# Kernel tuning notes

Hardware: AMD Instinct MI355X
Metric: run time of the kernel (lower is better)

Reference implementation:

```python
import jax, jax.numpy as jnp
import numpy as np

IN_F, OUT_F, K = 1024, 1024, 12
EPS = 1e-6


def setup_inputs() -> dict:
    key = jax.random.key(0)
    k1, k2, k3, k4 = jax.random.split(key, 4)
    x = jax.random.normal(k1, (4, 4096, IN_F), dtype=jnp.float32)
    # grid: linspace(-2,2,K) per feature + small noise so sort is nontrivial
    base = jnp.linspace(-2.0, 2.0, K, dtype=jnp.float32)
    grid = base[None, :] + 0.1 * jax.random.normal(k2, (IN_F, K), dtype=jnp.float32)
    coeffs = 0.1 * jax.random.normal(k3, (IN_F, K), dtype=jnp.float32)
    tangents = jnp.zeros((IN_F, K), dtype=jnp.float32)
    knot_alive = jnp.full((IN_F, K), 3.0, dtype=jnp.float32)
    kw1, kw2 = jax.random.split(k4)
    proj_w = jax.random.normal(kw1, (OUT_F, IN_F), dtype=jnp.float32) / np.sqrt(IN_F)
    proj_b = jnp.zeros((OUT_F,), dtype=jnp.float32)
    res_w = jax.random.normal(kw2, (OUT_F, IN_F), dtype=jnp.float32) / np.sqrt(IN_F)
    return {"x": x, "grid": grid, "coeffs": coeffs, "tangents": tangents,
            "knot_alive": knot_alive, "proj_w": proj_w, "proj_b": proj_b, "res_w": res_w}


def _eval_hermite_spline(x, grid, coeffs, tangents, knot_alive):
    # sort knots per input feature (grid: [F,K])
    sort_idx = jnp.argsort(grid, axis=1)
    sorted_grid = jnp.take_along_axis(grid, sort_idx, axis=1)
    sorted_coeffs = jnp.take_along_axis(coeffs, sort_idx, axis=1)
    sorted_tangents = jnp.take_along_axis(tangents, sort_idx, axis=1)
    sorted_alive = jnp.take_along_axis(knot_alive, sort_idx, axis=1)
    alive = jax.nn.sigmoid(sorted_alive)
    mc = sorted_coeffs * alive          # masked heights [F,K]
    mt = sorted_tangents * alive        # masked tangents [F,K]

    orig_shape = x.shape
    xf = x.reshape(-1, orig_shape[-1])  # [M,F]
    gmin = sorted_grid[:, 0]            # [F]
    gmax = sorted_grid[:, -1]
    xc = jnp.clip(xf, gmin[None, :], gmax[None, :])
    grange = jnp.maximum(gmax - gmin, EPS)
    xn = (xc - gmin[None, :]) / grange[None, :] * (K - 1)  # [M,F]
    idx_l = jnp.clip(xn.astype(jnp.int32), 0, K - 2)
    t = xn - idx_l.astype(xf.dtype)

    feat = jnp.arange(xf.shape[1])[None, :]  # [1,F] broadcast against [M,F] idx
    p0 = mc[feat, idx_l]
    p1 = mc[feat, idx_l + 1]
    m0 = mt[feat, idx_l]
    m1 = mt[feat, idx_l + 1]
    x_left = sorted_grid[feat, idx_l]
    x_right = sorted_grid[feat, idx_l + 1]
    dx = jnp.maximum(x_right - x_left, EPS)

    t2 = t * t
    t3 = t2 * t
    h00 = 2 * t3 - 3 * t2 + 1
    h10 = t3 - 2 * t2 + t
    h01 = -2 * t3 + 3 * t2
    h11 = t3 - t2
    out = h00 * p0 + h10 * m0 * dx + h01 * p1 + h11 * m1 * dx
    return out.reshape(orig_shape)


def reference(x, grid, coeffs, tangents, knot_alive, proj_w, proj_b, res_w):
    spline_out = _eval_hermite_spline(x, grid, coeffs, tangents, knot_alive)
    # proj(spline_out) + residual(x); torch Linear: y = x @ W.T + b
    return (jnp.einsum('...i,oi->...o', spline_out, proj_w) + proj_b
            + jnp.einsum('...i,oi->...o', x, res_w))
```

## Files before the change

### kernel.cpp

```cpp
#include <hip/hip_runtime.h>
#include <hip/hip_bf16.h>


#define IN_F   1024
#define OUT_F  1024
#define KNOTS  12
#define M_ROWS 16384
#define GK     2048

#define BM   256
#define BN   256
#define BKT  64
#define NTK  (GK / BKT)

typedef __attribute__((ext_vector_type(8))) __bf16 bf16x8;
typedef __attribute__((ext_vector_type(4))) float  f32x4;

__device__ __forceinline__ unsigned short f2bf(float v) {
    unsigned int u = __float_as_uint(v);
    u = (u + 0x7fffu + ((u >> 16) & 1u)) >> 16;
    return (unsigned short)u;
}

__device__ __forceinline__ void gload16(const void* g, void* l) {
    __builtin_amdgcn_global_load_lds(
        (const __attribute__((address_space(1))) void*)g,
        (__attribute__((address_space(3))) void*)l, 16, 0, 0);
}

__global__ __launch_bounds__(256) void prep_kernel(
    const float* __restrict__ grid, const float* __restrict__ coeffs,
    const float* __restrict__ tangents, const float* __restrict__ alive,
    float* __restrict__ gmin, float* __restrict__ scale, float4* __restrict__ H)
{
    int f = blockIdx.x * blockDim.x + threadIdx.x;
    if (f >= IN_F) return;
    float g[KNOTS], c[KNOTS], t[KNOTS], a[KNOTS];
    for (int i = 0; i < KNOTS; ++i) {
        g[i] = grid[f*KNOTS+i];  c[i] = coeffs[f*KNOTS+i];
        t[i] = tangents[f*KNOTS+i]; a[i] = alive[f*KNOTS+i];
    }
    for (int i = 1; i < KNOTS; ++i) {
        float gk=g[i], ck=c[i], tk=t[i], ak=a[i];
        int j = i-1;
        while (j >= 0 && g[j] > gk) { g[j+1]=g[j]; c[j+1]=c[j]; t[j+1]=t[j]; a[j+1]=a[j]; --j; }
        g[j+1]=gk; c[j+1]=ck; t[j+1]=tk; a[j+1]=ak;
    }
    float mcl[KNOTS], mtl[KNOTS];
    for (int i = 0; i < KNOTS; ++i) {
        float s = 1.f / (1.f + expf(-a[i]));
        mcl[i] = c[i]*s;  mtl[i] = t[i]*s;
    }
    gmin[f] = g[0];
    float grange = fmaxf(g[KNOTS-1] - g[0], 1e-6f);
    scale[f] = (float)(KNOTS-1) / grange;
    for (int k = 0; k < KNOTS-1; ++k) {
        float dx = fmaxf(g[k+1]-g[k], 1e-6f);
        H[(size_t)f*KNOTS + k] = make_float4(mcl[k], mcl[k+1], mtl[k]*dx, mtl[k+1]*dx);
    }
    H[(size_t)f*KNOTS + KNOTS-1] = make_float4(0.f, 0.f, 0.f, 0.f);
}

#define SROWS 64
#define HPAD  13
__global__ __launch_bounds__(256) void spline_kernel(const float* __restrict__ x,
    const float* __restrict__ gmin, const float* __restrict__ scale,
    const float4* __restrict__ H, unsigned short* __restrict__ A)
{
    __shared__ float4 sH[256 * HPAD];
    __shared__ float  sGm[256], sSc[256];
    const int tid  = threadIdx.x;
    const int fblk = blockIdx.y * 256;
    #pragma unroll
    for (int k = 0; k < KNOTS; ++k) sH[tid*HPAD + k] = H[(size_t)(fblk+tid)*KNOTS + k];
    sGm[tid] = gmin[fblk+tid];
    sSc[tid] = scale[fblk+tid];
    __syncthreads();

    const int wave = tid >> 6, lane = tid & 63;
    const int f0 = lane * 4;
    const float4 gm4 = *reinterpret_cast<const float4*>(&sGm[f0]);
    const float4 sc4 = *reinterpret_cast<const float4*>(&sSc[f0]);
    const float gms[4] = {gm4.x, gm4.y, gm4.z, gm4.w};
    const float scs[4] = {sc4.x, sc4.y, sc4.z, sc4.w};
    const int r0 = blockIdx.x * SROWS;

    #pragma unroll 8
    for (int r = wave; r < SROWS; r += 4) {
        const int row = r0 + r;
        const float4 xv = *reinterpret_cast<const float4*>(x + (size_t)row*IN_F + fblk + f0);
        const float xs[4] = {xv.x, xv.y, xv.z, xv.w};
        ushort4 so, xo;
        unsigned short* sp = (unsigned short*)&so;
        unsigned short* xp = (unsigned short*)&xo;
        #pragma unroll
        for (int j = 0; j < 4; ++j) {
            const float xi = xs[j];
            float xn = (xi - gms[j]) * scs[j];
            xn = fminf(fmaxf(xn, 0.f), (float)(KNOTS-1));
            int idx = (int)xn;  idx = idx > (KNOTS-2) ? (KNOTS-2) : idx;
            const float tt = xn - (float)idx;
            const float4 h = sH[(f0+j)*HPAD + idx];
            const float t2 = tt*tt, t3 = t2*tt;
            const float h00 =  2.f*t3 - 3.f*t2 + 1.f;
            const float h01 = -2.f*t3 + 3.f*t2;
            const float h10 =  t3 - 2.f*t2 + tt;
            const float h11 =  t3 - t2;
            sp[j] = f2bf(h00*h.x + h01*h.y + h10*h.z + h11*h.w);
            xp[j] = f2bf(xi);
        }
        const size_t base = (size_t)row * GK + fblk + f0;
        *reinterpret_cast<ushort4*>(A + base)        = so;
        *reinterpret_cast<ushort4*>(A + base + IN_F) = xo;
    }
}

__global__ __launch_bounds__(256) void bcast_kernel(
    const float* __restrict__ P, const float* __restrict__ R,
    unsigned short* __restrict__ Bc)
{
    int g = blockIdx.x*256 + threadIdx.x;
    int n  = g >> 9;
    int k4 = (g & 511) * 4;
    const float* src = (k4 < IN_F) ? (P + (size_t)n*IN_F + k4)
                                   : (R + (size_t)n*IN_F + (k4 - IN_F));
    float4 v = *reinterpret_cast<const float4*>(src);
    ushort4 o;
    o.x = f2bf(v.x); o.y = f2bf(v.y); o.z = f2bf(v.z); o.w = f2bf(v.w);
    *reinterpret_cast<ushort4*>(Bc + (size_t)n*GK + k4) = o;
}

__global__ __launch_bounds__(1024, 4) void gemm_kernel(
    const unsigned short* __restrict__ A, const unsigned short* __restrict__ B,
    const float* __restrict__ bias, float* __restrict__ C)
{
    __shared__ unsigned short sA[2][BM*BKT];
    __shared__ unsigned short sB[2][BN*BKT];

    const int tid  = threadIdx.x;
    const int wg   = blockIdx.x;
    const int swzb = (wg & 7) * 32 + (wg >> 3);
    const int by   = swzb >> 2;
    const int bx   = swzb & 3;

    const int lane = tid & 63;
    const int wave = tid >> 6;
    const int wm   = wave >> 2;
    const int wn   = wave & 3;
    const int lr   = lane & 15;
    const int lsl  = lane >> 4;

    const size_t aRow0 = (size_t)by * BM;
    const size_t bRow0 = (size_t)bx * BN;

    auto stage = [&](const unsigned short* __restrict__ G, size_t gRow0,
                     unsigned short* lds, int ts) {
        const int k0 = ts * BKT;
        #pragma unroll
        for (int i = 0; i < 2; ++i) {
            const int L16  = i*1024 + tid;
            const int lrow = L16 >> 3;
            const int ss   = (L16 & 7) ^ (lrow & 7);
            gload16(G + (gRow0 + lrow)*GK + k0 + ss*8, lds + (size_t)L16*8);
        }
    };
    auto rd = [&](const unsigned short* s, int lrow, int ks) -> bf16x8 {
        const int sp = (ks*4 + lsl) ^ (lrow & 7);
        return *reinterpret_cast<const bf16x8*>(s + lrow*BKT + sp*8);
    };

    f32x4 acc[4][4] = {};

    stage(A, aRow0, &sA[0][0], 0);
    stage(B, bRow0, &sB[0][0], 0);

    for (int t = 0; t < NTK; ++t) {
        const int b = t & 1;
        const unsigned short* cA = &sA[b][0];
        const unsigned short* cB = &sB[b][0];

        asm volatile("s_waitcnt vmcnt(0)" ::: "memory");
        __builtin_amdgcn_s_barrier();

        {
            bf16x8 av[4], bv[4];
            #pragma unroll
            for (int m = 0; m < 4; ++m) av[m] = rd(cA, wm*64 + m*16 + lr, 0);
            #pragma unroll
            for (int n = 0; n < 4; ++n) bv[n] = rd(cB, wn*64 + n*16 + lr, 0);
            if (t + 1 < NTK) {
                stage(A, aRow0, &sA[b^1][0], t+1);
                stage(B, bRow0, &sB[b^1][0], t+1);
            }
            __builtin_amdgcn_s_setprio(1);
            #pragma unroll
            for (int m = 0; m < 4; ++m)
              #pragma unroll
              for (int n = 0; n < 4; ++n)
                acc[m][n] = __builtin_amdgcn_mfma_f32_16x16x32_bf16(av[m], bv[n], acc[m][n], 0, 0, 0);
            __builtin_amdgcn_s_setprio(0);
        }
        {
            bf16x8 av[4], bv[4];
            #pragma unroll
            for (int m = 0; m < 4; ++m) av[m] = rd(cA, wm*64 + m*16 + lr, 1);
            #pragma unroll
            for (int n = 0; n < 4; ++n) bv[n] = rd(cB, wn*64 + n*16 + lr, 1);
            __builtin_amdgcn_s_setprio(1);
            #pragma unroll
            for (int m = 0; m < 4; ++m)
              #pragma unroll
              for (int n = 0; n < 4; ++n)
                acc[m][n] = __builtin_amdgcn_mfma_f32_16x16x32_bf16(av[m], bv[n], acc[m][n], 0, 0, 0);
            __builtin_amdgcn_s_setprio(0);
        }
    }

    #pragma unroll
    for (int n = 0; n < 4; ++n) {
        const int col = bx*BN + wn*64 + n*16 + lr;
        const float bv = bias[col];
        #pragma unroll
        for (int m = 0; m < 4; ++m) {
            const int grow = by*BM + wm*64 + m*16 + lsl*4;
            #pragma unroll
            for (int r = 0; r < 4; ++r)
                C[(size_t)(grow + r)*OUT_F + col] = acc[m][n][r] + bv;
        }
    }
}

__global__ __launch_bounds__(256) void fallback_kernel(
    const float* __restrict__ x, const float* __restrict__ P,
    const float* __restrict__ R, const float* __restrict__ pb,
    const float* __restrict__ gmin, const float* __restrict__ scale,
    const float4* __restrict__ H, float* __restrict__ out)
{
    __shared__ float s_s[IN_F];
    __shared__ float s_x[IN_F];
    int row = blockIdx.x;
    const float* xr = x + (size_t)row*IN_F;
    for (int f = threadIdx.x; f < IN_F; f += 256) {
        float xi = xr[f];
        float xn = (xi - gmin[f]) * scale[f];
        xn = fminf(fmaxf(xn, 0.f), (float)(KNOTS-1));
        int idx = (int)xn;  idx = idx > (KNOTS-2) ? (KNOTS-2) : idx;
        float tt = xn - (float)idx;
        float4 h = H[(size_t)f*KNOTS + idx];
        float t2 = tt*tt, t3 = t2*tt;
        s_s[f] = (2.f*t3-3.f*t2+1.f)*h.x + (-2.f*t3+3.f*t2)*h.y
               + (t3-2.f*t2+tt)*h.z + (t3-t2)*h.w;
        s_x[f] = xi;
    }
    __syncthreads();
    for (int j = 0; j < 4; ++j) {
        int o = threadIdx.x + j*256;
        const float* Pr = P + (size_t)o*IN_F;
        const float* Rr = R + (size_t)o*IN_F;
        float acc = pb[o];
        for (int f = 0; f < IN_F; ++f)
            acc = fmaf(s_s[f], Pr[f], fmaf(s_x[f], Rr[f], acc));
        out[(size_t)row*OUT_F + o] = acc;
    }
}

extern "C" void kernel_launch(void* const* d_in, const int* in_sizes, int n_in,
                              void* d_out, int out_size, void* d_ws, size_t ws_size,
                              hipStream_t stream) {
    const float* x         = (const float*)d_in[0];
    const float* grid      = (const float*)d_in[1];
    const float* coeffs    = (const float*)d_in[2];
    const float* tangents  = (const float*)d_in[3];
    const float* knotalive = (const float*)d_in[4];
    const float* proj_w    = (const float*)d_in[5];
    const float* proj_b    = (const float*)d_in[6];
    const float* res_w     = (const float*)d_in[7];
    float* out = (float*)d_out;

    const size_t needB  = (size_t)OUT_F * GK * 2;
    const size_t needA  = (size_t)M_ROWS * GK * 2;
    const size_t needT  = ((size_t)IN_F*2 + (size_t)IN_F*KNOTS*4) * 4;

    char* ws = (char*)d_ws;
    if (ws_size >= needB + needA + needT) {
        unsigned short* Bcat = (unsigned short*)ws;
        unsigned short* Abuf = (unsigned short*)(ws + needB);
        float*  gmin = (float*)(ws + needB + needA);
        float*  scl  = gmin + IN_F;
        float4* H    = (float4*)(scl + IN_F);

        prep_kernel<<<(IN_F+255)/256, 256, 0, stream>>>(grid, coeffs, tangents, knotalive,
                                                        gmin, scl, H);
        bcast_kernel<<<(OUT_F*GK/4)/256, 256, 0, stream>>>(proj_w, res_w, Bcat);
        spline_kernel<<<dim3(M_ROWS/SROWS, IN_F/256), 256, 0, stream>>>(x, gmin, scl, H, Abuf);
        gemm_kernel<<<(M_ROWS/BM)*(OUT_F/BN), 1024, 0, stream>>>(Abuf, Bcat, proj_b, out);
    } else {
        float*  gmin = (float*)ws;
        float*  scl  = gmin + IN_F;
        float4* H    = (float4*)(scl + IN_F);
        prep_kernel<<<(IN_F+255)/256, 256, 0, stream>>>(grid, coeffs, tangents, knotalive,
                                                        gmin, scl, H);
        fallback_kernel<<<M_ROWS, 256, 0, stream>>>(x, proj_w, res_w, proj_b,
                                                    gmin, scl, H, out);
    }
}
```

Measured before the change: 111.8 us.

## Fuse weight cast into prep kernel and store spline table in bf16

Merges the weight-concatenation bf16 cast with the knot preprocessing into one launch, so there is one fewer kernel launch. The Hermite segment table is also stored in bf16, which halves the spline kernel's LDS footprint, and a launch bound of 6 blocks per SM is added to raise occupancy. gmin and scale are now read directly from global memory instead of being staged in LDS. The bf16 table adds rounding error to the spline coefficients.

```diff
diff --git a/kernel.cpp b/kernel.cpp
--- a/kernel.cpp
+++ b/kernel.cpp
@@ -21,6 +21,9 @@
     u = (u + 0x7fffu + ((u >> 16) & 1u)) >> 16;
     return (unsigned short)u;
 }
+__device__ __forceinline__ float bf2f(unsigned short b) {
+    return __uint_as_float(((unsigned int)b) << 16);
+}
 
 __device__ __forceinline__ void gload16(const void* g, void* l) {
     __builtin_amdgcn_global_load_lds(
@@ -28,12 +31,28 @@
         (__attribute__((address_space(3))) void*)l, 16, 0, 0);
 }
 
-__global__ __launch_bounds__(256) void prep_kernel(
+__global__ __launch_bounds__(256) void prep_bcast_kernel(
     const float* __restrict__ grid, const float* __restrict__ coeffs,
     const float* __restrict__ tangents, const float* __restrict__ alive,
-    float* __restrict__ gmin, float* __restrict__ scale, float4* __restrict__ H)
-{
-    int f = blockIdx.x * blockDim.x + threadIdx.x;
+    const float* __restrict__ P, const float* __restrict__ R,
+    unsigned short* __restrict__ Bc,
+    float* __restrict__ gmin, float* __restrict__ scale,
+    float4* __restrict__ H, ushort4* __restrict__ Hb)
+{
+    const int blk = blockIdx.x;
+    if (blk < 2048) {
+        int g = blk*256 + threadIdx.x;
+        int n  = g >> 9;
+        int k4 = (g & 511) * 4;
+        const float* src = (k4 < IN_F) ? (P + (size_t)n*IN_F + k4)
+                                       : (R + (size_t)n*IN_F + (k4 - IN_F));
+        float4 v = *reinterpret_cast<const float4*>(src);
+        ushort4 o;
+        o.x = f2bf(v.x); o.y = f2bf(v.y); o.z = f2bf(v.z); o.w = f2bf(v.w);
+        *reinterpret_cast<ushort4*>(Bc + (size_t)n*GK + k4) = o;
+        return;
+    }
+    int f = (blk - 2048) * 256 + threadIdx.x;
     if (f >= IN_F) return;
     float g[KNOTS], c[KNOTS], t[KNOTS], a[KNOTS];
     for (int i = 0; i < KNOTS; ++i) {
@@ -56,31 +75,31 @@
     scale[f] = (float)(KNOTS-1) / grange;
     for (int k = 0; k < KNOTS-1; ++k) {
         float dx = fmaxf(g[k+1]-g[k], 1e-6f);
-        H[(size_t)f*KNOTS + k] = make_float4(mcl[k], mcl[k+1], mtl[k]*dx, mtl[k+1]*dx);
-    }
-    H[(size_t)f*KNOTS + KNOTS-1] = make_float4(0.f, 0.f, 0.f, 0.f);
+        float4 h = make_float4(mcl[k], mcl[k+1], mtl[k]*dx, mtl[k+1]*dx);
+        H[(size_t)f*KNOTS + k] = h;
+        Hb[(size_t)f*KNOTS + k] = make_ushort4(f2bf(h.x), f2bf(h.y), f2bf(h.z), f2bf(h.w));
+    }
+    H[(size_t)f*KNOTS + KNOTS-1]  = make_float4(0.f, 0.f, 0.f, 0.f);
+    Hb[(size_t)f*KNOTS + KNOTS-1] = make_ushort4(0, 0, 0, 0);
 }
 
 #define SROWS 64
 #define HPAD  13
-__global__ __launch_bounds__(256) void spline_kernel(const float* __restrict__ x,
+__global__ __launch_bounds__(256, 6) void spline_kernel(const float* __restrict__ x,
     const float* __restrict__ gmin, const float* __restrict__ scale,
-    const float4* __restrict__ H, unsigned short* __restrict__ A)
-{
-    __shared__ float4 sH[256 * HPAD];
-    __shared__ float  sGm[256], sSc[256];
+    const ushort4* __restrict__ Hb, unsigned short* __restrict__ A)
+{
+    __shared__ ushort4 sH[256 * HPAD];
     const int tid  = threadIdx.x;
     const int fblk = blockIdx.y * 256;
     #pragma unroll
-    for (int k = 0; k < KNOTS; ++k) sH[tid*HPAD + k] = H[(size_t)(fblk+tid)*KNOTS + k];
-    sGm[tid] = gmin[fblk+tid];
-    sSc[tid] = scale[fblk+tid];
+    for (int k = 0; k < KNOTS; ++k) sH[tid*HPAD + k] = Hb[(size_t)(fblk+tid)*KNOTS + k];
     __syncthreads();
 
     const int wave = tid >> 6, lane = tid & 63;
     const int f0 = lane * 4;
-    const float4 gm4 = *reinterpret_cast<const float4*>(&sGm[f0]);
-    const float4 sc4 = *reinterpret_cast<const float4*>(&sSc[f0]);
+    const float4 gm4 = *reinterpret_cast<const float4*>(gmin + fblk + f0);
+    const float4 sc4 = *reinterpret_cast<const float4*>(scale + fblk + f0);
     const float gms[4] = {gm4.x, gm4.y, gm4.z, gm4.w};
     const float scs[4] = {sc4.x, sc4.y, sc4.z, sc4.w};
     const int r0 = blockIdx.x * SROWS;
@@ -100,34 +119,20 @@
             xn = fminf(fmaxf(xn, 0.f), (float)(KNOTS-1));
             int idx = (int)xn;  idx = idx > (KNOTS-2) ? (KNOTS-2) : idx;
             const float tt = xn - (float)idx;
-            const float4 h = sH[(f0+j)*HPAD + idx];
+            const ushort4 hb = sH[(f0+j)*HPAD + idx];
+            const float hx = bf2f(hb.x), hy = bf2f(hb.y), hz = bf2f(hb.z), hw = bf2f(hb.w);
             const float t2 = tt*tt, t3 = t2*tt;
             const float h00 =  2.f*t3 - 3.f*t2 + 1.f;
             const float h01 = -2.f*t3 + 3.f*t2;
             const float h10 =  t3 - 2.f*t2 + tt;
             const float h11 =  t3 - t2;
-            sp[j] = f2bf(h00*h.x + h01*h.y + h10*h.z + h11*h.w);
+            sp[j] = f2bf(h00*hx + h01*hy + h10*hz + h11*hw);
             xp[j] = f2bf(xi);
         }
         const size_t base = (size_t)row * GK + fblk + f0;
         *reinterpret_cast<ushort4*>(A + base)        = so;
         *reinterpret_cast<ushort4*>(A + base + IN_F) = xo;
     }
-}
-
-__global__ __launch_bounds__(256) void bcast_kernel(
-    const float* __restrict__ P, const float* __restrict__ R,
-    unsigned short* __restrict__ Bc)
-{
-    int g = blockIdx.x*256 + threadIdx.x;
-    int n  = g >> 9;
-    int k4 = (g & 511) * 4;
-    const float* src = (k4 < IN_F) ? (P + (size_t)n*IN_F + k4)
-                                   : (R + (size_t)n*IN_F + (k4 - IN_F));
-    float4 v = *reinterpret_cast<const float4*>(src);
-    ushort4 o;
-    o.x = f2bf(v.x); o.y = f2bf(v.y); o.z = f2bf(v.z); o.w = f2bf(v.w);
-    *reinterpret_cast<ushort4*>(Bc + (size_t)n*GK + k4) = o;
 }
 
 __global__ __launch_bounds__(1024, 4) void gemm_kernel(
@@ -228,6 +233,39 @@
                 C[(size_t)(grow + r)*OUT_F + col] = acc[m][n][r] + bv;
         }
     }
+}
+
+__global__ __launch_bounds__(256) void fallback_prep_kernel(
+    const float* __restrict__ grid, const float* __restrict__ coeffs,
+    const float* __restrict__ tangents, const float* __restrict__ alive,
+    float* __restrict__ gmin, float* __restrict__ scale, float4* __restrict__ H)
+{
+    int f = blockIdx.x * blockDim.x + threadIdx.x;
+    if (f >= IN_F) return;
+    float g[KNOTS], c[KNOTS], t[KNOTS], a[KNOTS];
+    for (int i = 0; i < KNOTS; ++i) {
+        g[i] = grid[f*KNOTS+i];  c[i] = coeffs[f*KNOTS+i];
+        t[i] = tangents[f*KNOTS+i]; a[i] = alive[f*KNOTS+i];
+    }
+    for (int i = 1; i < KNOTS; ++i) {
+        float gk=g[i], ck=c[i], tk=t[i], ak=a[i];
+        int j = i-1;
+        while (j >= 0 && g[j] > gk) { g[j+1]=g[j]; c[j+1]=c[j]; t[j+1]=t[j]; a[j+1]=a[j]; --j; }
+        g[j+1]=gk; c[j+1]=ck; t[j+1]=tk; a[j+1]=ak;
+    }
+    float mcl[KNOTS], mtl[KNOTS];
+    for (int i = 0; i < KNOTS; ++i) {
+        float s = 1.f / (1.f + expf(-a[i]));
+        mcl[i] = c[i]*s;  mtl[i] = t[i]*s;
+    }
+    gmin[f] = g[0];
+    float grange = fmaxf(g[KNOTS-1] - g[0], 1e-6f);
+    scale[f] = (float)(KNOTS-1) / grange;
+    for (int k = 0; k < KNOTS-1; ++k) {
+        float dx = fmaxf(g[k+1]-g[k], 1e-6f);
+        H[(size_t)f*KNOTS + k] = make_float4(mcl[k], mcl[k+1], mtl[k]*dx, mtl[k+1]*dx);
+    }
+    H[(size_t)f*KNOTS + KNOTS-1] = make_float4(0.f, 0.f, 0.f, 0.f);
 }
 
 __global__ __launch_bounds__(256) void fallback_kernel(
@@ -279,27 +317,28 @@
 
     const size_t needB  = (size_t)OUT_F * GK * 2;
     const size_t needA  = (size_t)M_ROWS * GK * 2;
-    const size_t needT  = ((size_t)IN_F*2 + (size_t)IN_F*KNOTS*4) * 4;
+    const size_t needT  = ((size_t)IN_F*2 + (size_t)IN_F*KNOTS*4) * 4
+                        + (size_t)IN_F*KNOTS*8;
 
     char* ws = (char*)d_ws;
     if (ws_size >= needB + needA + needT) {
         unsigned short* Bcat = (unsigned short*)ws;
         unsigned short* Abuf = (unsigned short*)(ws + needB);
-        float*  gmin = (float*)(ws + needB + needA);
-        float*  scl  = gmin + IN_F;
-        float4* H    = (float4*)(scl + IN_F);
-
-        prep_kernel<<<(IN_F+255)/256, 256, 0, stream>>>(grid, coeffs, tangents, knotalive,
-                                                        gmin, scl, H);
-        bcast_kernel<<<(OUT_F*GK/4)/256, 256, 0, stream>>>(proj_w, res_w, Bcat);
-        spline_kernel<<<dim3(M_ROWS/SROWS, IN_F/256), 256, 0, stream>>>(x, gmin, scl, H, Abuf);
+        float*   gmin = (float*)(ws + needB + needA);
+        float*   scl  = gmin + IN_F;
+        float4*  H    = (float4*)(scl + IN_F);
+        ushort4* Hb   = (ushort4*)(H + (size_t)IN_F*KNOTS);
+
+        prep_bcast_kernel<<<2048 + IN_F/256, 256, 0, stream>>>(
+            grid, coeffs, tangents, knotalive, proj_w, res_w, Bcat, gmin, scl, H, Hb);
+        spline_kernel<<<dim3(M_ROWS/SROWS, IN_F/256), 256, 0, stream>>>(x, gmin, scl, Hb, Abuf);
         gemm_kernel<<<(M_ROWS/BM)*(OUT_F/BN), 1024, 0, stream>>>(Abuf, Bcat, proj_b, out);
     } else {
         float*  gmin = (float*)ws;
         float*  scl  = gmin + IN_F;
         float4* H    = (float4*)(scl + IN_F);
-        prep_kernel<<<(IN_F+255)/256, 256, 0, stream>>>(grid, coeffs, tangents, knotalive,
-                                                        gmin, scl, H);
+        fallback_prep_kernel<<<(IN_F+255)/256, 256, 0, stream>>>(grid, coeffs, tangents, knotalive,
+                                                                 gmin, scl, H);
         fallback_kernel<<<M_ROWS, 256, 0, stream>>>(x, proj_w, res_w, proj_b,
                                                     gmin, scl, H, out);
     }
```

Result: faster. 102.1 us (median of 2 runs) (-8.6%).
